# Optimization experiments

Hardware: AMD Instinct MI355X
Metric: run time of the kernel (lower is better)

Reference implementation:

```python
import jax, jax.numpy as jnp
import numpy as np

NUM_EXPERTS = 8
TOP_K = 2
HIDDEN = 1024
INTER_TOTAL = 8192  # intermediate_size * experts_per_rank
B, S = 2, 2048


def setup_inputs() -> dict:
    key = jax.random.key(0)
    k1, k2, k3, k4, k5, k6 = jax.random.split(key, 6)
    T = B * S
    x = jax.random.normal(k1, (B, S, HIDDEN), dtype=jnp.float32)
    scores = jax.random.uniform(k2, (T, NUM_EXPERTS), dtype=jnp.float32)
    expert_weights = jax.random.uniform(k3, (T, TOP_K), dtype=jnp.float32)
    top_experts = jax.random.randint(k4, (T, TOP_K), 0, NUM_EXPERTS, dtype=jnp.int32)
    w1 = jax.random.normal(k5, (HIDDEN, INTER_TOTAL), dtype=jnp.float32) * 0.02
    w2 = jax.random.normal(k6, (INTER_TOTAL, HIDDEN), dtype=jnp.float32) * 0.02
    return {"x": x, "scores": scores, "expert_weights": expert_weights,
            "top_experts": top_experts, "w1": w1, "w2": w2}


def reference(x, scores, expert_weights, top_experts, w1, w2):
    # forward_once with expert_parallel_size == 1 (dropless MoE dispatch/combine).
    in_shape = x.shape
    T = in_shape[0] * in_shape[1]
    H = in_shape[-1]
    x_flat = x.reshape(T, H)

    flat_experts = top_experts.reshape(-1)          # [T*top_k]
    flat_weights = expert_weights.reshape(-1)       # [T*top_k]

    # ops.sort: stable radix sort of routed copies by expert id
    order = jnp.argsort(flat_experts, stable=True)  # "indices"
    token_idx = order // TOP_K                      # source token per sorted slot

    # padded_gather: bucket tokens per expert (padding rows are zeros and
    # pass through the bias-free MLP as zeros, so they never affect output)
    xg = x_flat[token_idx]                          # [T*top_k, H]

    # MLP: w1 -> gelu(tanh approx) -> w2
    h = jax.nn.gelu(xg @ w1, approximate=True)      # [T*top_k, inter*E]
    y = h @ w2                                      # [T*top_k, H]

    # padded_scatter: weighted combine back to token order
    w_sorted = flat_weights[order]
    out = jnp.zeros((T, H), dtype=x.dtype).at[token_idx].add(w_sorted[:, None] * y)
    return out.reshape(in_shape)
```

## Files before the change

### kernel.cpp

```cpp
#include <hip/hip_runtime.h>
#include <hip/hip_bf16.h>
#include <math.h>

#define HID 1024
#define INTER 8192
#define TT 4096

typedef __bf16 bf16x8 __attribute__((ext_vector_type(8)));
typedef float f32x4 __attribute__((ext_vector_type(4)));

__device__ __forceinline__ void gll16(const void* g, void* l) {
    __builtin_amdgcn_global_load_lds(
        (const __attribute__((address_space(1))) void*)g,
        (__attribute__((address_space(3))) void*)l, 16, 0, 0);
}

__global__ void k_prep(const float* __restrict__ x, const float* __restrict__ ew,
                       __hip_bfloat16* __restrict__ xb, float* __restrict__ s,
                       int n4, int T) {
    int stride = gridDim.x * blockDim.x;
    for (int i = blockIdx.x * blockDim.x + threadIdx.x; i < n4; i += stride) {
        float4 v = ((const float4*)x)[i];
        __hip_bfloat16* o = xb + (size_t)i * 4;
        o[0] = __float2bfloat16(v.x);
        o[1] = __float2bfloat16(v.y);
        o[2] = __float2bfloat16(v.z);
        o[3] = __float2bfloat16(v.w);
    }
    for (int t = blockIdx.x * blockDim.x + threadIdx.x; t < T; t += stride)
        s[t] = ew[2 * t] + ew[2 * t + 1];
}

__global__ void k_tcast(const float* __restrict__ in, __hip_bfloat16* __restrict__ out,
                        int R, int C) {
    __shared__ float tile[32][33];
    const int tx = threadIdx.x & 31, ty = threadIdx.x >> 5;
    const int br = blockIdx.y * 32, bc = blockIdx.x * 32;
#pragma unroll
    for (int j = 0; j < 32; j += 8)
        tile[ty + j][tx] = in[(size_t)(br + ty + j) * C + bc + tx];
    __syncthreads();
#pragma unroll
    for (int j = 0; j < 32; j += 8)
        out[(size_t)(bc + ty + j) * R + br + tx] = __float2bfloat16(tile[tx][ty + j]);
}

template <int EPI>
__global__ __launch_bounds__(512, 2) void k_gemm8(
    const __hip_bfloat16* __restrict__ A, const __hip_bfloat16* __restrict__ Bt,
    __hip_bfloat16* __restrict__ hOut, float* __restrict__ fOut,
    const float* __restrict__ s, int Kfull, int nt, int Nout) {
    __shared__ __hip_bfloat16 sA[2][2][128][64];
    __shared__ __hip_bfloat16 sB[2][2][128][64];
    const int tid = threadIdx.x;
    const int lane = tid & 63, wid = tid >> 6;
    const int wr = wid >> 2, wc = wid & 3;

    const int nwg = gridDim.x * gridDim.y;
    const int wg = blockIdx.y * gridDim.x + blockIdx.x;
    const int swz = (wg & 7) * (nwg >> 3) + (wg >> 3);
    const int brow = (swz / gridDim.x) * 256;
    const int bcol = (swz % gridDim.x) * 256;
    const size_t kbase = (size_t)blockIdx.z * ((size_t)nt * 64);

    const int rstage = tid >> 3;
    const int colsw = (((tid & 7) ^ (rstage & 7)) << 3);
    const __hip_bfloat16* gA = A + (size_t)(brow + rstage) * Kfull + kbase + colsw;
    const __hip_bfloat16* gB = Bt + (size_t)(bcol + rstage) * Kfull + kbase + colsw;
    const size_t rowStep = (size_t)64 * Kfull;
    const size_t halfStep = (size_t)128 * Kfull;

    char* ldsA0 = (char*)&sA[0][0][0][0] + wid * 1024;
    char* ldsB0 = (char*)&sB[0][0][0][0] + wid * 1024;

    const int g0 = (((lane >> 4)) ^ (lane & 7)) << 4;
    const int g1 = ((4 + (lane >> 4)) ^ (lane & 7)) << 4;
    const char* rdA = (const char*)&sA[0][wr][0][0] + (lane & 15) * 128;
    const char* rdB = (const char*)&sB[0][wc >> 1][0][0] + (wc & 1) * 8192 + (lane & 15) * 128;

    f32x4 acc[8][4] = {};
    bf16x8 aF[4][2], b01[2][2], b23[2][2];

#define STAGE_A(buf, half, t)                                              \
    do {                                                                   \
        const __hip_bfloat16* _g = gA + (half) * halfStep + (size_t)(t) * 64; \
        char* _l = ldsA0 + (buf) * 32768 + (half) * 16384;                 \
        gll16(_g, _l);                                                     \
        gll16(_g + rowStep, _l + 8192);                                    \
    } while (0)
#define STAGE_B(buf, half, t)                                              \
    do {                                                                   \
        const __hip_bfloat16* _g = gB + (half) * halfStep + (size_t)(t) * 64; \
        char* _l = ldsB0 + (buf) * 32768 + (half) * 16384;                 \
        gll16(_g, _l);                                                     \
        gll16(_g + rowStep, _l + 8192);                                    \
    } while (0)
#define PIN() __builtin_amdgcn_sched_barrier(0)
#define BAR()                              \
    do {                                   \
        PIN();                             \
        __builtin_amdgcn_s_barrier();      \
        PIN();                             \
    } while (0)
#define WAIT_LGKM0() __builtin_amdgcn_s_waitcnt(0xC07F)
#define WAIT_LGKM8() __builtin_amdgcn_s_waitcnt(0xC87F)
#define WAIT_VM4() __builtin_amdgcn_s_waitcnt(0x0F74)
#define WAIT_VM0() __builtin_amdgcn_s_waitcnt(0x0F70)
#define RD(base, buf, r2048, ks) \
    (*(const bf16x8*)((base) + (buf) * 32768 + (r2048) * 2048 + ((ks) ? g1 : g0)))
#define MM_Q(mbase, nbase, bfr)                                                   \
    _Pragma("unroll") for (int ks = 0; ks < 2; ++ks)                              \
    _Pragma("unroll") for (int m = 0; m < 4; ++m)                                 \
    _Pragma("unroll") for (int n = 0; n < 2; ++n)                                 \
        acc[(mbase) + m][(nbase) + n] = __builtin_amdgcn_mfma_f32_16x16x32_bf16(  \
            aF[m][ks], bfr[n][ks], acc[(mbase) + m][(nbase) + n], 0, 0, 0);
#define MFMA_PHASE(mbase, nbase, bfr)     \
    do {                                  \
        WAIT_LGKM0();                     \
        PIN();                            \
        __builtin_amdgcn_s_setprio(1);    \
        MM_Q(mbase, nbase, bfr);          \
        __builtin_amdgcn_s_setprio(0);    \
        PIN();                            \
    } while (0)

    STAGE_B(0, 0, 0);
    STAGE_B(0, 1, 0);
    STAGE_A(0, 0, 0);
    STAGE_A(0, 1, 0);
    STAGE_B(1, 0, 1);
    STAGE_B(1, 1, 1);
    WAIT_VM4();
    BAR();

    const int iters = nt >> 1;
    for (int i = 0; i < iters; ++i) {
        const bool full = (i + 1 < iters);
        const int t1 = 2 * i + 1, t2 = 2 * i + 2, t3 = 2 * i + 3;

#pragma unroll
        for (int m = 0; m < 4; ++m) {
            aF[m][0] = RD(rdA, 0, m, 0);
            aF[m][1] = RD(rdA, 0, m, 1);
        }
#pragma unroll
        for (int n = 0; n < 2; ++n) {
            b01[n][0] = RD(rdB, 0, n, 0);
            b01[n][1] = RD(rdB, 0, n, 1);
        }
        STAGE_A(1, 0, t1);
        WAIT_LGKM8();
        BAR();
        MFMA_PHASE(0, 0, b01);
        BAR();

#pragma unroll
        for (int n = 0; n < 2; ++n) {
            b23[n][0] = RD(rdB, 0, 2 + n, 0);
            b23[n][1] = RD(rdB, 0, 2 + n, 1);
        }
        STAGE_A(1, 1, t1);
        BAR();
        MFMA_PHASE(0, 2, b23);
        BAR();

#pragma unroll
        for (int m = 0; m < 4; ++m) {
            aF[m][0] = RD(rdA, 0, 4 + m, 0);
            aF[m][1] = RD(rdA, 0, 4 + m, 1);
        }
        if (full) STAGE_B(0, 0, t2);
        BAR();
        MFMA_PHASE(4, 2, b23);
        BAR();

        if (full) STAGE_B(0, 1, t2);
        BAR();
        MFMA_PHASE(4, 0, b01);
        if (full)
            WAIT_VM4();
        else
            WAIT_VM0();
        BAR();

#pragma unroll
        for (int m = 0; m < 4; ++m) {
            aF[m][0] = RD(rdA, 1, m, 0);
            aF[m][1] = RD(rdA, 1, m, 1);
        }
#pragma unroll
        for (int n = 0; n < 2; ++n) {
            b01[n][0] = RD(rdB, 1, n, 0);
            b01[n][1] = RD(rdB, 1, n, 1);
        }
        if (full) STAGE_A(0, 0, t2);
        WAIT_LGKM8();
        BAR();
        MFMA_PHASE(0, 0, b01);
        BAR();

#pragma unroll
        for (int n = 0; n < 2; ++n) {
            b23[n][0] = RD(rdB, 1, 2 + n, 0);
            b23[n][1] = RD(rdB, 1, 2 + n, 1);
        }
        if (full) STAGE_A(0, 1, t2);
        BAR();
        MFMA_PHASE(0, 2, b23);
        BAR();

#pragma unroll
        for (int m = 0; m < 4; ++m) {
            aF[m][0] = RD(rdA, 1, 4 + m, 0);
            aF[m][1] = RD(rdA, 1, 4 + m, 1);
        }
        if (full) STAGE_B(1, 0, t3);
        BAR();
        MFMA_PHASE(4, 2, b23);
        BAR();

        if (full) STAGE_B(1, 1, t3);
        BAR();
        MFMA_PHASE(4, 0, b01);
        if (full)
            WAIT_VM4();
        else
            WAIT_VM0();
        BAR();
    }

    const int orow = brow + wr * 128 + ((lane >> 4) << 2);
    const int ocol = bcol + wc * 64 + (lane & 15);
#pragma unroll
    for (int m = 0; m < 8; ++m) {
#pragma unroll
        for (int j = 0; j < 4; ++j) {
            const int r = orow + m * 16 + j;
            const size_t ro = (size_t)r * Nout;
            if (EPI == 0) {
#pragma unroll
                for (int n = 0; n < 4; ++n) {
                    float v = acc[m][n][j];
                    float u = 1.5957691216057308f * (v + 0.044715f * v * v * v);
                    float g = v / (1.0f + __expf(-u));
                    hOut[ro + ocol + n * 16] = __float2bfloat16(g);
                }
            } else {
                const float sc = s[r];
#pragma unroll
                for (int n = 0; n < 4; ++n)
                    unsafeAtomicAdd(&fOut[ro + ocol + n * 16], sc * acc[m][n][j]);
            }
        }
    }
#undef STAGE_A
#undef STAGE_B
#undef PIN
#undef BAR
#undef WAIT_LGKM0
#undef WAIT_LGKM8
#undef WAIT_VM4
#undef WAIT_VM0
#undef RD
#undef MM_Q
#undef MFMA_PHASE
}

extern "C" void kernel_launch(void* const* d_in, const int* in_sizes, int n_in,
                              void* d_out, int out_size, void* d_ws, size_t ws_size,
                              hipStream_t stream) {
    const float* x = (const float*)d_in[0];
    const float* ew = (const float*)d_in[2];
    const float* w1 = (const float*)d_in[4];
    const float* w2 = (const float*)d_in[5];
    float* out = (float*)d_out;

    char* ws = (char*)d_ws;
    float* s = (float*)ws;
    __hip_bfloat16* xb = (__hip_bfloat16*)(ws + 16384);
    __hip_bfloat16* w1t = (__hip_bfloat16*)(ws + 16384 + 8388608);
    __hip_bfloat16* w2t = (__hip_bfloat16*)(ws + 16384 + 8388608 + 16777216);
    __hip_bfloat16* h = (__hip_bfloat16*)(ws + 16384 + 8388608 + 2 * 16777216);

    k_prep<<<1024, 256, 0, stream>>>(x, ew, xb, s, (TT * HID) / 4, TT);

    dim3 t1(INTER / 32, HID / 32);
    k_tcast<<<t1, 256, 0, stream>>>(w1, w1t, HID, INTER);
    dim3 t2(HID / 32, INTER / 32);
    k_tcast<<<t2, 256, 0, stream>>>(w2, w2t, INTER, HID);

    dim3 g1(INTER / 256, TT / 256, 1);
    k_gemm8<0><<<g1, 512, 0, stream>>>(xb, w1t, h, nullptr, nullptr, HID, HID / 64, INTER);

    hipMemsetAsync(out, 0, (size_t)TT * HID * sizeof(float), stream);
    dim3 g2(HID / 256, TT / 256, 4);
    k_gemm8<1><<<g2, 512, 0, stream>>>(h, w2t, nullptr, out, s, INTER, 2048 / 64, HID);
}
```

Baseline: 228.6 us.

## Fuse prep and weight transpose kernels; give GEMM1 workgroups two column tiles

The x cast, the routing-weight sum and both weight transpose-casts now run in a single launch, with block ranges dispatched by block id, which removes two kernel launches and their gaps. The first GEMM gets a CSEG template parameter so each workgroup loops over two adjacent 256-column tiles serially, halving its grid from 512 to 256 workgroups. That is roughly one wave on a 256-CU part and avoids a partial second wave, at the cost of longer per-workgroup runtime and no overlap between the two segments' prologue and epilogue.

```diff
diff --git a/kernel.cpp b/kernel.cpp
--- a/kernel.cpp
+++ b/kernel.cpp
@@ -15,27 +15,12 @@
         (__attribute__((address_space(3))) void*)l, 16, 0, 0);
 }
 
-__global__ void k_prep(const float* __restrict__ x, const float* __restrict__ ew,
-                       __hip_bfloat16* __restrict__ xb, float* __restrict__ s,
-                       int n4, int T) {
-    int stride = gridDim.x * blockDim.x;
-    for (int i = blockIdx.x * blockDim.x + threadIdx.x; i < n4; i += stride) {
-        float4 v = ((const float4*)x)[i];
-        __hip_bfloat16* o = xb + (size_t)i * 4;
-        o[0] = __float2bfloat16(v.x);
-        o[1] = __float2bfloat16(v.y);
-        o[2] = __float2bfloat16(v.z);
-        o[3] = __float2bfloat16(v.w);
-    }
-    for (int t = blockIdx.x * blockDim.x + threadIdx.x; t < T; t += stride)
-        s[t] = ew[2 * t] + ew[2 * t + 1];
-}
-
-__global__ void k_tcast(const float* __restrict__ in, __hip_bfloat16* __restrict__ out,
-                        int R, int C) {
+__device__ __forceinline__ void tcast_tile(const float* __restrict__ in,
+                                           __hip_bfloat16* __restrict__ out,
+                                           int R, int C, int bx, int by, int tid) {
     __shared__ float tile[32][33];
-    const int tx = threadIdx.x & 31, ty = threadIdx.x >> 5;
-    const int br = blockIdx.y * 32, bc = blockIdx.x * 32;
+    const int tx = tid & 31, ty = tid >> 5;
+    const int br = by * 32, bc = bx * 32;
 #pragma unroll
     for (int j = 0; j < 32; j += 8)
         tile[ty + j][tx] = in[(size_t)(br + ty + j) * C + bc + tx];
@@ -45,7 +30,34 @@
         out[(size_t)(bc + ty + j) * R + br + tx] = __float2bfloat16(tile[tx][ty + j]);
 }
 
-template <int EPI>
+__global__ void k_prep(const float* __restrict__ x, const float* __restrict__ ew,
+                       const float* __restrict__ w1, const float* __restrict__ w2,
+                       __hip_bfloat16* __restrict__ xb, float* __restrict__ s,
+                       __hip_bfloat16* __restrict__ w1t, __hip_bfloat16* __restrict__ w2t) {
+    const int bid = blockIdx.x, tid = threadIdx.x;
+    if (bid < 1024) {
+        const int n4 = (TT * HID) / 4;
+        const int stride = 1024 * 256;
+        for (int i = bid * 256 + tid; i < n4; i += stride) {
+            float4 v = ((const float4*)x)[i];
+            __hip_bfloat16* o = xb + (size_t)i * 4;
+            o[0] = __float2bfloat16(v.x);
+            o[1] = __float2bfloat16(v.y);
+            o[2] = __float2bfloat16(v.z);
+            o[3] = __float2bfloat16(v.w);
+        }
+        for (int t = bid * 256 + tid; t < TT; t += stride)
+            s[t] = ew[2 * t] + ew[2 * t + 1];
+    } else if (bid < 1024 + 8192) {
+        const int b = bid - 1024;
+        tcast_tile(w1, w1t, HID, INTER, b % 256, b / 256, tid);
+    } else {
+        const int b = bid - (1024 + 8192);
+        tcast_tile(w2, w2t, INTER, HID, b % 32, b / 32, tid);
+    }
+}
+
+template <int EPI, int CSEG>
 __global__ __launch_bounds__(512, 2) void k_gemm8(
     const __hip_bfloat16* __restrict__ A, const __hip_bfloat16* __restrict__ Bt,
     __hip_bfloat16* __restrict__ hOut, float* __restrict__ fOut,
@@ -60,13 +72,13 @@
     const int wg = blockIdx.y * gridDim.x + blockIdx.x;
     const int swz = (wg & 7) * (nwg >> 3) + (wg >> 3);
     const int brow = (swz / gridDim.x) * 256;
-    const int bcol = (swz % gridDim.x) * 256;
+    const int bcol0 = (swz % gridDim.x) * (256 * CSEG);
     const size_t kbase = (size_t)blockIdx.z * ((size_t)nt * 64);
 
     const int rstage = tid >> 3;
     const int colsw = (((tid & 7) ^ (rstage & 7)) << 3);
     const __hip_bfloat16* gA = A + (size_t)(brow + rstage) * Kfull + kbase + colsw;
-    const __hip_bfloat16* gB = Bt + (size_t)(bcol + rstage) * Kfull + kbase + colsw;
+    const __hip_bfloat16* gB0 = Bt + (size_t)(bcol0 + rstage) * Kfull + kbase + colsw;
     const size_t rowStep = (size_t)64 * Kfull;
     const size_t halfStep = (size_t)128 * Kfull;
 
@@ -77,9 +89,6 @@
     const int g1 = ((4 + (lane >> 4)) ^ (lane & 7)) << 4;
     const char* rdA = (const char*)&sA[0][wr][0][0] + (lane & 15) * 128;
     const char* rdB = (const char*)&sB[0][wc >> 1][0][0] + (wc & 1) * 8192 + (lane & 15) * 128;
-
-    f32x4 acc[8][4] = {};
-    bf16x8 aF[4][2], b01[2][2], b23[2][2];
 
 #define STAGE_A(buf, half, t)                                              \
     do {                                                                   \
@@ -90,7 +99,7 @@
     } while (0)
 #define STAGE_B(buf, half, t)                                              \
     do {                                                                   \
-        const __hip_bfloat16* _g = gB + (half) * halfStep + (size_t)(t) * 64; \
+        const __hip_bfloat16* _g = gBc + (half) * halfStep + (size_t)(t) * 64; \
         char* _l = ldsB0 + (buf) * 32768 + (half) * 16384;                 \
         gll16(_g, _l);                                                     \
         gll16(_g + rowStep, _l + 8192);                                    \
@@ -124,132 +133,141 @@
         PIN();                            \
     } while (0)
 
-    STAGE_B(0, 0, 0);
-    STAGE_B(0, 1, 0);
-    STAGE_A(0, 0, 0);
-    STAGE_A(0, 1, 0);
-    STAGE_B(1, 0, 1);
-    STAGE_B(1, 1, 1);
-    WAIT_VM4();
-    BAR();
-
-    const int iters = nt >> 1;
-    for (int i = 0; i < iters; ++i) {
-        const bool full = (i + 1 < iters);
-        const int t1 = 2 * i + 1, t2 = 2 * i + 2, t3 = 2 * i + 3;
-
-#pragma unroll
-        for (int m = 0; m < 4; ++m) {
-            aF[m][0] = RD(rdA, 0, m, 0);
-            aF[m][1] = RD(rdA, 0, m, 1);
+#pragma unroll 1
+    for (int cs = 0; cs < CSEG; ++cs) {
+        const __hip_bfloat16* gBc = gB0 + (size_t)cs * 256 * Kfull;
+        const int bcol = bcol0 + cs * 256;
+
+        f32x4 acc[8][4] = {};
+        bf16x8 aF[4][2], b01[2][2], b23[2][2];
+
+        STAGE_B(0, 0, 0);
+        STAGE_B(0, 1, 0);
+        STAGE_A(0, 0, 0);
+        STAGE_A(0, 1, 0);
+        STAGE_B(1, 0, 1);
+        STAGE_B(1, 1, 1);
+        WAIT_VM4();
+        BAR();
+
+        const int iters = nt >> 1;
+        for (int i = 0; i < iters; ++i) {
+            const bool full = (i + 1 < iters);
+            const int t1 = 2 * i + 1, t2 = 2 * i + 2, t3 = 2 * i + 3;
+
+#pragma unroll
+            for (int m = 0; m < 4; ++m) {
+                aF[m][0] = RD(rdA, 0, m, 0);
+                aF[m][1] = RD(rdA, 0, m, 1);
+            }
+#pragma unroll
+            for (int n = 0; n < 2; ++n) {
+                b01[n][0] = RD(rdB, 0, n, 0);
+                b01[n][1] = RD(rdB, 0, n, 1);
+            }
+            STAGE_A(1, 0, t1);
+            WAIT_LGKM8();
+            BAR();
+            MFMA_PHASE(0, 0, b01);
+            BAR();
+
+#pragma unroll
+            for (int n = 0; n < 2; ++n) {
+                b23[n][0] = RD(rdB, 0, 2 + n, 0);
+                b23[n][1] = RD(rdB, 0, 2 + n, 1);
+            }
+            STAGE_A(1, 1, t1);
+            BAR();
+            MFMA_PHASE(0, 2, b23);
+            BAR();
+
+#pragma unroll
+            for (int m = 0; m < 4; ++m) {
+                aF[m][0] = RD(rdA, 0, 4 + m, 0);
+                aF[m][1] = RD(rdA, 0, 4 + m, 1);
+            }
+            if (full) STAGE_B(0, 0, t2);
+            BAR();
+            MFMA_PHASE(4, 2, b23);
+            BAR();
+
+            if (full) STAGE_B(0, 1, t2);
+            BAR();
+            MFMA_PHASE(4, 0, b01);
+            if (full)
+                WAIT_VM4();
+            else
+                WAIT_VM0();
+            BAR();
+
+#pragma unroll
+            for (int m = 0; m < 4; ++m) {
+                aF[m][0] = RD(rdA, 1, m, 0);
+                aF[m][1] = RD(rdA, 1, m, 1);
+            }
+#pragma unroll
+            for (int n = 0; n < 2; ++n) {
+                b01[n][0] = RD(rdB, 1, n, 0);
+                b01[n][1] = RD(rdB, 1, n, 1);
+            }
+            if (full) STAGE_A(0, 0, t2);
+            WAIT_LGKM8();
+            BAR();
+            MFMA_PHASE(0, 0, b01);
+            BAR();
+
+#pragma unroll
+            for (int n = 0; n < 2; ++n) {
+                b23[n][0] = RD(rdB, 1, 2 + n, 0);
+                b23[n][1] = RD(rdB, 1, 2 + n, 1);
+            }
+            if (full) STAGE_A(0, 1, t2);
+            BAR();
+            MFMA_PHASE(0, 2, b23);
+            BAR();
+
+#pragma unroll
+            for (int m = 0; m < 4; ++m) {
+                aF[m][0] = RD(rdA, 1, 4 + m, 0);
+                aF[m][1] = RD(rdA, 1, 4 + m, 1);
+            }
+            if (full) STAGE_B(1, 0, t3);
+            BAR();
+            MFMA_PHASE(4, 2, b23);
+            BAR();
+
+            if (full) STAGE_B(1, 1, t3);
+            BAR();
+            MFMA_PHASE(4, 0, b01);
+            if (full)
+                WAIT_VM4();
+            else
+                WAIT_VM0();
+            BAR();
         }
-#pragma unroll
-        for (int n = 0; n < 2; ++n) {
-            b01[n][0] = RD(rdB, 0, n, 0);
-            b01[n][1] = RD(rdB, 0, n, 1);
-        }
-        STAGE_A(1, 0, t1);
-        WAIT_LGKM8();
-        BAR();
-        MFMA_PHASE(0, 0, b01);
-        BAR();
-
-#pragma unroll
-        for (int n = 0; n < 2; ++n) {
-            b23[n][0] = RD(rdB, 0, 2 + n, 0);
-            b23[n][1] = RD(rdB, 0, 2 + n, 1);
-        }
-        STAGE_A(1, 1, t1);
-        BAR();
-        MFMA_PHASE(0, 2, b23);
-        BAR();
-
-#pragma unroll
-        for (int m = 0; m < 4; ++m) {
-            aF[m][0] = RD(rdA, 0, 4 + m, 0);
-            aF[m][1] = RD(rdA, 0, 4 + m, 1);
-        }
-        if (full) STAGE_B(0, 0, t2);
-        BAR();
-        MFMA_PHASE(4, 2, b23);
-        BAR();
-
-        if (full) STAGE_B(0, 1, t2);
-        BAR();
-        MFMA_PHASE(4, 0, b01);
-        if (full)
-            WAIT_VM4();
-        else
-            WAIT_VM0();
-        BAR();
-
-#pragma unroll
-        for (int m = 0; m < 4; ++m) {
-            aF[m][0] = RD(rdA, 1, m, 0);
-            aF[m][1] = RD(rdA, 1, m, 1);
-        }
-#pragma unroll
-        for (int n = 0; n < 2; ++n) {
-            b01[n][0] = RD(rdB, 1, n, 0);
-            b01[n][1] = RD(rdB, 1, n, 1);
-        }
-        if (full) STAGE_A(0, 0, t2);
-        WAIT_LGKM8();
-        BAR();
-        MFMA_PHASE(0, 0, b01);
-        BAR();
-
-#pragma unroll
-        for (int n = 0; n < 2; ++n) {
-            b23[n][0] = RD(rdB, 1, 2 + n, 0);
-            b23[n][1] = RD(rdB, 1, 2 + n, 1);
-        }
-        if (full) STAGE_A(0, 1, t2);
-        BAR();
-        MFMA_PHASE(0, 2, b23);
-        BAR();
-
-#pragma unroll
-        for (int m = 0; m < 4; ++m) {
-            aF[m][0] = RD(rdA, 1, 4 + m, 0);
-            aF[m][1] = RD(rdA, 1, 4 + m, 1);
-        }
-        if (full) STAGE_B(1, 0, t3);
-        BAR();
-        MFMA_PHASE(4, 2, b23);
-        BAR();
-
-        if (full) STAGE_B(1, 1, t3);
-        BAR();
-        MFMA_PHASE(4, 0, b01);
-        if (full)
-            WAIT_VM4();
-        else
-            WAIT_VM0();
-        BAR();
-    }
-
-    const int orow = brow + wr * 128 + ((lane >> 4) << 2);
-    const int ocol = bcol + wc * 64 + (lane & 15);
-#pragma unroll
-    for (int m = 0; m < 8; ++m) {
-#pragma unroll
-        for (int j = 0; j < 4; ++j) {
-            const int r = orow + m * 16 + j;
-            const size_t ro = (size_t)r * Nout;
-            if (EPI == 0) {
-#pragma unroll
-                for (int n = 0; n < 4; ++n) {
-                    float v = acc[m][n][j];
-                    float u = 1.5957691216057308f * (v + 0.044715f * v * v * v);
-                    float g = v / (1.0f + __expf(-u));
-                    hOut[ro + ocol + n * 16] = __float2bfloat16(g);
+
+        const int orow = brow + wr * 128 + ((lane >> 4) << 2);
+        const int ocol = bcol + wc * 64 + (lane & 15);
+#pragma unroll
+        for (int m = 0; m < 8; ++m) {
+#pragma unroll
+            for (int j = 0; j < 4; ++j) {
+                const int r = orow + m * 16 + j;
+                const size_t ro = (size_t)r * Nout;
+                if (EPI == 0) {
+#pragma unroll
+                    for (int n = 0; n < 4; ++n) {
+                        float v = acc[m][n][j];
+                        float u = 1.5957691216057308f * (v + 0.044715f * v * v * v);
+                        float g = v / (1.0f + __expf(-u));
+                        hOut[ro + ocol + n * 16] = __float2bfloat16(g);
+                    }
+                } else {
+                    const float sc = s[r];
+#pragma unroll
+                    for (int n = 0; n < 4; ++n)
+                        unsafeAtomicAdd(&fOut[ro + ocol + n * 16], sc * acc[m][n][j]);
                 }
-            } else {
-                const float sc = s[r];
-#pragma unroll
-                for (int n = 0; n < 4; ++n)
-                    unsafeAtomicAdd(&fOut[ro + ocol + n * 16], sc * acc[m][n][j]);
             }
         }
     }
@@ -282,17 +300,12 @@
     __hip_bfloat16* w2t = (__hip_bfloat16*)(ws + 16384 + 8388608 + 16777216);
     __hip_bfloat16* h = (__hip_bfloat16*)(ws + 16384 + 8388608 + 2 * 16777216);
 
-    k_prep<<<1024, 256, 0, stream>>>(x, ew, xb, s, (TT * HID) / 4, TT);
-
-    dim3 t1(INTER / 32, HID / 32);
-    k_tcast<<<t1, 256, 0, stream>>>(w1, w1t, HID, INTER);
-    dim3 t2(HID / 32, INTER / 32);
-    k_tcast<<<t2, 256, 0, stream>>>(w2, w2t, INTER, HID);
-
-    dim3 g1(INTER / 256, TT / 256, 1);
-    k_gemm8<0><<<g1, 512, 0, stream>>>(xb, w1t, h, nullptr, nullptr, HID, HID / 64, INTER);
+    k_prep<<<1024 + 8192 + 8192, 256, 0, stream>>>(x, ew, w1, w2, xb, s, w1t, w2t);
+
+    dim3 g1(INTER / 512, TT / 256, 1);
+    k_gemm8<0, 2><<<g1, 512, 0, stream>>>(xb, w1t, h, nullptr, nullptr, HID, HID / 64, INTER);
 
     hipMemsetAsync(out, 0, (size_t)TT * HID * sizeof(float), stream);
     dim3 g2(HID / 256, TT / 256, 4);
-    k_gemm8<1><<<g2, 512, 0, stream>>>(h, w2t, nullptr, out, s, INTER, 2048 / 64, HID);
-}
+    k_gemm8<1, 1><<<g2, 512, 0, stream>>>(h, w2t, nullptr, out, s, INTER, 2048 / 64, HID);
+}
```

Result: slower. 234.8 us (+2.7%).
